# Kernel optimization log

Hardware: AMD Instinct MI355X
Metric: run time of the kernel (lower is better)

The kernel has to match this reference:

```python
import jax, jax.numpy as jnp
import numpy as np

HUMAN_SIZE = 54
NUM_ACTIONS = 15
INPUT_SIZE = HUMAN_SIZE + NUM_ACTIONS  # 69
RNN_SIZE = 2048
BATCH = 512
SRC_LEN = 100
TGT_LEN = 50


def setup_inputs() -> dict:
    key = jax.random.key(0)
    ks = jax.random.split(key, 8)
    s = 1.0 / np.sqrt(RNN_SIZE)
    return {
        "encoder_inputs": jax.random.normal(ks[0], (BATCH, SRC_LEN, INPUT_SIZE), jnp.float32),
        "decoder_inputs": jax.random.normal(ks[1], (BATCH, TGT_LEN, INPUT_SIZE), jnp.float32),
        # GRUCell params (torch layout: weight_ih [3H, D], weight_hh [3H, H])
        "W_ih": jax.random.uniform(ks[2], (3 * RNN_SIZE, INPUT_SIZE), jnp.float32, -s, s),
        "W_hh": jax.random.uniform(ks[3], (3 * RNN_SIZE, RNN_SIZE), jnp.float32, -s, s),
        "b_ih": jax.random.uniform(ks[4], (3 * RNN_SIZE,), jnp.float32, -s, s),
        "b_hh": jax.random.uniform(ks[5], (3 * RNN_SIZE,), jnp.float32, -s, s),
        # fc1: Linear(rnn_size -> input_size)
        "fc1_w": jax.random.uniform(ks[6], (INPUT_SIZE, RNN_SIZE), jnp.float32, -s, s),
        "fc1_b": jax.random.uniform(ks[7], (INPUT_SIZE,), jnp.float32, -s, s),
    }


def _gru_cell(x, h, W_ih, W_hh, b_ih, b_hh):
    # torch.nn.GRUCell math
    gi = x @ W_ih.T + b_ih  # [B, 3H]
    gh = h @ W_hh.T + b_hh  # [B, 3H]
    i_r, i_z, i_n = jnp.split(gi, 3, axis=-1)
    h_r, h_z, h_n = jnp.split(gh, 3, axis=-1)
    r = jax.nn.sigmoid(i_r + h_r)
    z = jax.nn.sigmoid(i_z + h_z)
    n = jnp.tanh(i_n + r * h_n)
    return (1.0 - z) * n + z * h


def reference(encoder_inputs, decoder_inputs, W_ih, W_hh, b_ih, b_hh, fc1_w, fc1_b):
    B = encoder_inputs.shape[0]
    state0 = jnp.zeros((B, RNN_SIZE), encoder_inputs.dtype)

    # Encoder: source_seq_len - 1 steps (dropout p=0.0 -> identity)
    enc_t = jnp.swapaxes(encoder_inputs[:, : SRC_LEN - 1], 0, 1)  # [L-1, B, D]

    def enc_step(h, x):
        return _gru_cell(x, h, W_ih, W_hh, b_ih, b_hh), None

    state, _ = jax.lax.scan(enc_step, state0, enc_t)

    # (loop_function feeds the previous output back as the next input).
    def dec_step(carry, _):
        h, inp = carry
        inp = jax.lax.stop_gradient(inp)  # inp.detach() in torch
        h = _gru_cell(inp, h, W_ih, W_hh, b_ih, b_hh)
        out = inp + h @ fc1_w.T + fc1_b  # residual
        return (h, out), out

    (_, _), outs = jax.lax.scan(dec_step, (state, decoder_inputs[:, 0]), None, length=TGT_LEN)
    return jnp.swapaxes(outs, 0, 1)  # [B, TGT_LEN, INPUT_SIZE]
```

## Files before the change

### kernel.cpp

```cpp
#include <hip/hip_runtime.h>

#define KP   2176
#define H    2048
#define MB   512
#define IN   69
#define TGT  50

typedef unsigned short ushort_t;
typedef __attribute__((ext_vector_type(8))) short  short8;
typedef __attribute__((ext_vector_type(4))) float  float4_t;

__device__ __forceinline__ ushort_t f2bf(float f) {
  union { float f; unsigned u; } v; v.f = f;
  unsigned u = v.u;
  return (ushort_t)((u + 0x7fffu + ((u >> 16) & 1u)) >> 16);
}

__device__ __forceinline__ void gload_lds16(const void* g, void* l) {
  __builtin_amdgcn_global_load_lds((const __attribute__((address_space(1))) void*)g,
                                   (__attribute__((address_space(3))) void*)l, 16, 0, 0);
}

template <int N> __device__ __forceinline__ void waitv() {
  asm volatile("s_waitcnt vmcnt(%0)" :: "n"(N) : "memory");
}


__global__ void build_wbig(const float* __restrict__ Whh, const float* __restrict__ Wih,
                           ushort_t* __restrict__ Wbig) {
  int k = blockIdx.x * 256 + threadIdx.x;
  int n = blockIdx.y;
  if (k >= KP) return;
  int g = (n >> 6) % 3;
  int c = (n / 192) * 64 + (n & 63);
  int gr = g * H + c;
  float v = 0.f;
  if (k < H) v = Whh[(size_t)gr * H + k];
  else if (k < H + IN) v = Wih[(size_t)gr * IN + (k - H)];
  Wbig[(size_t)n * KP + k] = f2bf(v);
}

__global__ void zero_u4(uint4* p, int n) {
  int i = blockIdx.x * 256 + threadIdx.x;
  if (i < n) p[i] = make_uint4(0, 0, 0, 0);
}

__global__ void fill_x0(const float* __restrict__ enc, ushort_t* __restrict__ Acat0) {
  int i = blockIdx.x * 256 + threadIdx.x;
  int b = i / IN, j = i - b * IN;
  Acat0[(size_t)b * KP + H + j] = f2bf(enc[(size_t)b * 100 * IN + j]);
}

__global__ void build_fc1(const float* __restrict__ fc1w, ushort_t* __restrict__ fc1b16) {
  int k = blockIdx.x * 256 + threadIdx.x;
  int n = blockIdx.y;
  float v = (n < IN) ? fc1w[(size_t)n * H + k] : 0.f;
  fc1b16[(size_t)n * H + k] = f2bf(v);
}

__global__ __launch_bounds__(256, 1) void gru_step(
    const ushort_t* __restrict__ Aprev, ushort_t* __restrict__ Anext,
    const ushort_t* __restrict__ Wbig, float* __restrict__ h32,
    const float* __restrict__ b_ih, const float* __restrict__ b_hh,
    const float* __restrict__ xsrc, int xstride)
{
  __shared__ __align__(16) char lds[4][32768];

  const int tid = threadIdx.x;
  const int bid = blockIdx.x;
  const int xcd = bid & 7, slot = bid >> 3;
  const int ct = xcd * 4 + (slot & 3);
  const int mt = slot >> 2;
  const int m0 = mt * 64, c0 = ct * 64;
  const int lane = tid & 63, w = tid >> 6;
  const int l15 = lane & 15, l4 = lane >> 4;

  const ushort_t* srcA[2];
  const ushort_t* srcB[6];
  #pragma unroll
  for (int r = 0; r < 2; ++r) {
    int byte = r * 4096 + tid * 16;
    int row = byte >> 7, colb = byte & 127;
    int sc = colb ^ ((row & 7) << 4);
    srcA[r] = Aprev + (size_t)(m0 + row) * KP + (sc >> 1);
  }
  #pragma unroll
  for (int r = 0; r < 6; ++r) {
    int byte = r * 4096 + tid * 16;
    int row = byte >> 7, colb = byte & 127;
    int sc = colb ^ ((row & 7) << 4);
    srcB[r] = Wbig + (size_t)(ct * 192 + row) * KP + (sc >> 1);
  }

  int offA[2][4], offB[2][3];
  #pragma unroll
  for (int kk = 0; kk < 2; ++kk) {
    int kbyte = kk * 64 + l4 * 16;
    #pragma unroll
    for (int mi = 0; mi < 4; ++mi) { int row = mi * 16 + l15; offA[kk][mi] = row * 128 + (kbyte ^ ((row & 7) << 4)); }
    #pragma unroll
    for (int ni = 0; ni < 3; ++ni) { int row = ni * 64 + w * 16 + l15; offB[kk][ni] = row * 128 + (kbyte ^ ((row & 7) << 4)); }
  }

  float4_t acc[4][4] = {};

  auto stage = [&](int kt, int buf) {
    const int kadv = kt * 64;
    char* base = &lds[0][0] + buf * 32768;
    #pragma unroll
    for (int r = 0; r < 2; ++r)
      gload_lds16(srcA[r] + kadv, base + r * 4096 + w * 1024);
    #pragma unroll
    for (int r = 0; r < 6; ++r)
      gload_lds16(srcB[r] + kadv, base + 8192 + r * 4096 + w * 1024);
  };

  auto compute = [&](int buf, bool g3) {
    const char* Ab = (const char*)&lds[0][0] + buf * 32768;
    const char* Bb = Ab + 8192;
    #pragma unroll
    for (int kk = 0; kk < 2; ++kk) {
      short8 a[4], b[3];
      #pragma unroll
      for (int mi = 0; mi < 4; ++mi) a[mi] = *(const short8*)(Ab + offA[kk][mi]);
      #pragma unroll
      for (int ni = 0; ni < 3; ++ni) b[ni] = *(const short8*)(Bb + offB[kk][ni]);
      #pragma unroll
      for (int mi = 0; mi < 4; ++mi) {
        acc[mi][0] = __builtin_amdgcn_mfma_f32_16x16x32_bf16(a[mi], b[0], acc[mi][0], 0, 0, 0);
        acc[mi][1] = __builtin_amdgcn_mfma_f32_16x16x32_bf16(a[mi], b[1], acc[mi][1], 0, 0, 0);
        if (!g3)
          acc[mi][2] = __builtin_amdgcn_mfma_f32_16x16x32_bf16(a[mi], b[2], acc[mi][2], 0, 0, 0);
        else
          acc[mi][3] = __builtin_amdgcn_mfma_f32_16x16x32_bf16(a[mi], b[2], acc[mi][3], 0, 0, 0);
      }
    }
  };

  #define BAR() __builtin_amdgcn_s_barrier()

  stage(0, 0); stage(1, 1); stage(2, 2);
  for (int kt = 0; kt < 28; kt += 4) {
    waitv<16>(); BAR(); compute(0, false); stage(kt + 3, 3);
    waitv<16>(); BAR(); compute(1, false); stage(kt + 4, 0);
    waitv<16>(); BAR(); compute(2, false); stage(kt + 5, 1);
    waitv<16>(); BAR(); compute(3, false); stage(kt + 6, 2);
  }
  waitv<16>(); BAR(); compute(0, false); stage(31, 3);
  waitv<16>(); BAR(); compute(1, false); stage(32, 0);
  waitv<16>(); BAR(); compute(2, false); stage(33, 1);
  waitv<16>(); BAR(); compute(3, false);
  waitv<8>();  BAR(); compute(0, true);
  waitv<0>();  BAR(); compute(1, true);

  const int c = c0 + w * 16 + l15;
  const float br  = b_ih[c] + b_hh[c];
  const float bz  = b_ih[H + c] + b_hh[H + c];
  const float bin = b_ih[2 * H + c];
  const float bhn = b_hh[2 * H + c];
  #pragma unroll
  for (int mi = 0; mi < 4; ++mi) {
    #pragma unroll
    for (int r4 = 0; r4 < 4; ++r4) {
      int m = m0 + mi * 16 + l4 * 4 + r4;
      float rg = 1.f / (1.f + __expf(-(acc[mi][0][r4] + br)));
      float zg = 1.f / (1.f + __expf(-(acc[mi][1][r4] + bz)));
      float ng = tanhf(acc[mi][3][r4] + bin + rg * (acc[mi][2][r4] + bhn));
      float hold = h32[(size_t)m * H + c];
      float hn = (1.f - zg) * ng + zg * hold;
      h32[(size_t)m * H + c] = hn;
      Anext[(size_t)m * KP + c] = f2bf(hn);
    }
  }
  if (ct == 0 && xsrc != nullptr) {
    for (int i = tid; i < 64 * IN; i += 256) {
      int rr = i / IN, cc = i - rr * IN;
      Anext[(size_t)(m0 + rr) * KP + H + cc] = f2bf(xsrc[(size_t)(m0 + rr) * xstride + cc]);
    }
  }
}

__global__ __launch_bounds__(256, 1) void out_step(
    ushort_t* Acat,
    const ushort_t* __restrict__ fc1b16,
    const float* __restrict__ fc1_bias,
    const float* __restrict__ inp,
    float* __restrict__ outp)
{
  __shared__ __align__(16) char lds[4][20480];
  const int tid = threadIdx.x;
  const int m0 = blockIdx.x * 64;
  const int lane = tid & 63, w = tid >> 6, l15 = lane & 15, l4 = lane >> 4;

  const ushort_t* srcA[2]; const ushort_t* srcB[3];
  #pragma unroll
  for (int r = 0; r < 2; ++r) {
    int byte = r * 4096 + tid * 16; int row = byte >> 7, colb = byte & 127;
    int sc = colb ^ ((row & 7) << 4);
    srcA[r] = Acat + (size_t)(m0 + row) * KP + (sc >> 1);
  }
  #pragma unroll
  for (int r = 0; r < 3; ++r) {
    int byte = r * 4096 + tid * 16; int row = byte >> 7, colb = byte & 127;
    int sc = colb ^ ((row & 7) << 4);
    srcB[r] = fc1b16 + (size_t)row * H + (sc >> 1);
  }
  int offA[2], offB[2][5];
  #pragma unroll
  for (int kk = 0; kk < 2; ++kk) {
    int kbyte = kk * 64 + l4 * 16;
    { int row = w * 16 + l15; offA[kk] = row * 128 + (kbyte ^ ((row & 7) << 4)); }
    #pragma unroll
    for (int ni = 0; ni < 5; ++ni) { int row = ni * 16 + l15; offB[kk][ni] = row * 128 + (kbyte ^ ((row & 7) << 4)); }
  }

  float4_t acc[5] = {};
  auto stage = [&](int kt, int buf) {
    int kadv = kt * 64;
    char* base = &lds[0][0] + buf * 20480;
    #pragma unroll
    for (int r = 0; r < 2; ++r) gload_lds16(srcA[r] + kadv, base + r * 4096 + w * 1024);
    #pragma unroll
    for (int r = 0; r < 3; ++r) gload_lds16(srcB[r] + kadv, base + 8192 + r * 4096 + w * 1024);
  };
  auto compute = [&](int buf) {
    const char* Ab = (const char*)&lds[0][0] + buf * 20480;
    const char* Bb = Ab + 8192;
    #pragma unroll
    for (int kk = 0; kk < 2; ++kk) {
      short8 a = *(const short8*)(Ab + offA[kk]);
      #pragma unroll
      for (int ni = 0; ni < 5; ++ni) {
        short8 b = *(const short8*)(Bb + offB[kk][ni]);
        acc[ni] = __builtin_amdgcn_mfma_f32_16x16x32_bf16(a, b, acc[ni], 0, 0, 0);
      }
    }
  };

  stage(0, 0); stage(1, 1); stage(2, 2);
  for (int kt = 0; kt < 28; kt += 4) {
    waitv<10>(); BAR(); compute(0); stage(kt + 3, 3);
    waitv<10>(); BAR(); compute(1); stage(kt + 4, 0);
    waitv<10>(); BAR(); compute(2); stage(kt + 5, 1);
    waitv<10>(); BAR(); compute(3); stage(kt + 6, 2);
  }
  waitv<10>(); BAR(); compute(0); stage(31, 3);
  waitv<10>(); BAR(); compute(1);
  waitv<5>();  BAR(); compute(2);
  waitv<0>();  BAR(); compute(3);

  #pragma unroll
  for (int ni = 0; ni < 5; ++ni) {
    int j = ni * 16 + l15;
    if (j < IN) {
      float bj = fc1_bias[j];
      #pragma unroll
      for (int r4 = 0; r4 < 4; ++r4) {
        int m = m0 + w * 16 + l4 * 4 + r4;
        float v = acc[ni][r4] + bj + inp[(size_t)m * (TGT * IN) + j];
        outp[(size_t)m * (TGT * IN) + j] = v;
        Acat[(size_t)m * KP + H + j] = f2bf(v);
      }
    }
  }
}

extern "C" void kernel_launch(void* const* d_in, const int* in_sizes, int n_in,
                              void* d_out, int out_size, void* d_ws, size_t ws_size,
                              hipStream_t stream) {
  const float* enc  = (const float*)d_in[0];
  const float* dec  = (const float*)d_in[1];
  const float* Wih  = (const float*)d_in[2];
  const float* Whh  = (const float*)d_in[3];
  const float* b_ih = (const float*)d_in[4];
  const float* b_hh = (const float*)d_in[5];
  const float* fc1w = (const float*)d_in[6];
  const float* fc1b = (const float*)d_in[7];
  float* out = (float*)d_out;

  char* ws = (char*)d_ws;
  ushort_t* Wbig   = (ushort_t*)(ws);
  ushort_t* Acat0  = (ushort_t*)(ws + 26738688);
  ushort_t* Acat1  = (ushort_t*)(ws + 28966912);
  float*    h32    = (float*)   (ws + 31195136);
  ushort_t* fc1b16 = (ushort_t*)(ws + 35389440);
  ushort_t* Acat[2] = {Acat0, Acat1};

  build_wbig<<<dim3(9, 6144), 256, 0, stream>>>(Whh, Wih, Wbig);
  zero_u4<<<2112, 256, 0, stream>>>((uint4*)Acat0, 540672);
  fill_x0<<<138, 256, 0, stream>>>(enc, Acat0);
  build_fc1<<<dim3(8, 96), 256, 0, stream>>>(fc1w, fc1b16);

  for (int t = 0; t < 149; ++t) {
    const float* xsrc = nullptr; int xstride = 0;
    if (t < 98)       { xsrc = enc + (size_t)(t + 1) * IN; xstride = 100 * IN; }
    else if (t == 98) { xsrc = dec;                        xstride = TGT * IN; }
    gru_step<<<256, 256, 0, stream>>>(Acat[t & 1], Acat[(t + 1) & 1], Wbig, h32,
                                      b_ih, b_hh, xsrc, xstride);
    if (t >= 99) {
      int d = t - 99;
      const float* inp = (d == 0) ? dec : out + (size_t)(d - 1) * IN;
      out_step<<<8, 256, 0, stream>>>(Acat[(t + 1) & 1], fc1b16, fc1b, inp,
                                      out + (size_t)d * IN);
    }
  }
}
```

Measured before the change: 4.275 ms.

## Retile GRU step to 128x96 blocks with register double-buffered fragments

Changes the per-block tile from 64 rows by 192 gate columns to 128 rows by 96 gate columns, with waves split 2x2 over the M and column dimensions, and reorders the packed weight layout to match. The LDS pipeline now prefetches MFMA fragments into two register sets, so LDS reads for the next k-tile overlap the MFMAs of the current one, with an explicit lgkmcnt wait before each barrier. The aim is a more balanced A/B load ratio per block and hiding LDS read latency. In exchange it uses more registers and tightens the pipeline's wait counts.

Result: no change. 4.354 ms (+1.8%).

```diff
diff --git a/kernel.cpp b/kernel.cpp
--- a/kernel.cpp
+++ b/kernel.cpp
@@ -2,7 +2,6 @@
 
 #define KP   2176
 #define H    2048
-#define MB   512
 #define IN   69
 #define TGT  50
 
@@ -24,6 +23,8 @@
 template <int N> __device__ __forceinline__ void waitv() {
   asm volatile("s_waitcnt vmcnt(%0)" :: "n"(N) : "memory");
 }
+#define LGKM0() asm volatile("s_waitcnt lgkmcnt(0)" ::: "memory")
+#define BAR()   __builtin_amdgcn_s_barrier()
 
 
 __global__ void build_wbig(const float* __restrict__ Whh, const float* __restrict__ Wih,
@@ -31,9 +32,9 @@
   int k = blockIdx.x * 256 + threadIdx.x;
   int n = blockIdx.y;
   if (k >= KP) return;
-  int g = (n >> 6) % 3;
-  int c = (n / 192) * 64 + (n & 63);
-  int gr = g * H + c;
+  int ct = n / 96, rem = n - ct * 96;
+  int g = rem >> 5, c32 = rem & 31;
+  int gr = g * H + ct * 32 + c32;
   float v = 0.f;
   if (k < H) v = Whh[(size_t)gr * H + k];
   else if (k < H + IN) v = Wih[(size_t)gr * IN + (k - H)];
@@ -57,6 +58,8 @@
   float v = (n < IN) ? fc1w[(size_t)n * H + k] : 0.f;
   fc1b16[(size_t)n * H + k] = f2bf(v);
 }
+
+struct Frag { short8 a[2][4]; short8 b[2][3]; };
 
 __global__ __launch_bounds__(256, 1) void gru_step(
     const ushort_t* __restrict__ Aprev, ushort_t* __restrict__ Anext,
@@ -64,32 +67,33 @@
     const float* __restrict__ b_ih, const float* __restrict__ b_hh,
     const float* __restrict__ xsrc, int xstride)
 {
-  __shared__ __align__(16) char lds[4][32768];
+  __shared__ __align__(16) char lds[4][28672];
 
   const int tid = threadIdx.x;
   const int bid = blockIdx.x;
   const int xcd = bid & 7, slot = bid >> 3;
-  const int ct = xcd * 4 + (slot & 3);
-  const int mt = slot >> 2;
-  const int m0 = mt * 64, c0 = ct * 64;
+  const int ct = xcd * 8 + (slot & 7);
+  const int mt = slot >> 3;
+  const int m0 = mt * 128;
   const int lane = tid & 63, w = tid >> 6;
   const int l15 = lane & 15, l4 = lane >> 4;
-
-  const ushort_t* srcA[2];
-  const ushort_t* srcB[6];
-  #pragma unroll
-  for (int r = 0; r < 2; ++r) {
+  const int wm = w & 1, wc = w >> 1;
+
+  const ushort_t* srcA[4];
+  const ushort_t* srcB[3];
+  #pragma unroll
+  for (int r = 0; r < 4; ++r) {
     int byte = r * 4096 + tid * 16;
     int row = byte >> 7, colb = byte & 127;
     int sc = colb ^ ((row & 7) << 4);
     srcA[r] = Aprev + (size_t)(m0 + row) * KP + (sc >> 1);
   }
   #pragma unroll
-  for (int r = 0; r < 6; ++r) {
+  for (int r = 0; r < 3; ++r) {
     int byte = r * 4096 + tid * 16;
     int row = byte >> 7, colb = byte & 127;
     int sc = colb ^ ((row & 7) << 4);
-    srcB[r] = Wbig + (size_t)(ct * 192 + row) * KP + (sc >> 1);
+    srcB[r] = Wbig + (size_t)(ct * 96 + row) * KP + (sc >> 1);
   }
 
   int offA[2][4], offB[2][3];
@@ -97,63 +101,81 @@
   for (int kk = 0; kk < 2; ++kk) {
     int kbyte = kk * 64 + l4 * 16;
     #pragma unroll
-    for (int mi = 0; mi < 4; ++mi) { int row = mi * 16 + l15; offA[kk][mi] = row * 128 + (kbyte ^ ((row & 7) << 4)); }
-    #pragma unroll
-    for (int ni = 0; ni < 3; ++ni) { int row = ni * 64 + w * 16 + l15; offB[kk][ni] = row * 128 + (kbyte ^ ((row & 7) << 4)); }
+    for (int mi = 0; mi < 4; ++mi) {
+      int row = wm * 64 + mi * 16 + l15;
+      offA[kk][mi] = row * 128 + (kbyte ^ ((row & 7) << 4));
+    }
+    #pragma unroll
+    for (int g = 0; g < 3; ++g) {
+      int row = g * 32 + wc * 16 + l15;
+      offB[kk][g] = 16384 + row * 128 + (kbyte ^ ((row & 7) << 4));
+    }
   }
 
   float4_t acc[4][4] = {};
+  Frag F0, F1;
 
   auto stage = [&](int kt, int buf) {
     const int kadv = kt * 64;
-    char* base = &lds[0][0] + buf * 32768;
-    #pragma unroll
-    for (int r = 0; r < 2; ++r)
+    char* base = &lds[0][0] + buf * 28672;
+    #pragma unroll
+    for (int r = 0; r < 4; ++r)
       gload_lds16(srcA[r] + kadv, base + r * 4096 + w * 1024);
     #pragma unroll
-    for (int r = 0; r < 6; ++r)
-      gload_lds16(srcB[r] + kadv, base + 8192 + r * 4096 + w * 1024);
-  };
-
-  auto compute = [&](int buf, bool g3) {
-    const char* Ab = (const char*)&lds[0][0] + buf * 32768;
-    const char* Bb = Ab + 8192;
+    for (int r = 0; r < 3; ++r)
+      gload_lds16(srcB[r] + kadv, base + 16384 + r * 4096 + w * 1024);
+  };
+
+  auto dsread = [&](Frag& f, int buf) {
+    const char* base = (const char*)&lds[0][0] + buf * 28672;
     #pragma unroll
     for (int kk = 0; kk < 2; ++kk) {
-      short8 a[4], b[3];
-      #pragma unroll
-      for (int mi = 0; mi < 4; ++mi) a[mi] = *(const short8*)(Ab + offA[kk][mi]);
-      #pragma unroll
-      for (int ni = 0; ni < 3; ++ni) b[ni] = *(const short8*)(Bb + offB[kk][ni]);
+      #pragma unroll
+      for (int mi = 0; mi < 4; ++mi) f.a[kk][mi] = *(const short8*)(base + offA[kk][mi]);
+      #pragma unroll
+      for (int g = 0; g < 3; ++g)   f.b[kk][g]  = *(const short8*)(base + offB[kk][g]);
+    }
+  };
+
+  auto domfma = [&](Frag& f, int g3) {
+    #pragma unroll
+    for (int kk = 0; kk < 2; ++kk) {
       #pragma unroll
       for (int mi = 0; mi < 4; ++mi) {
-        acc[mi][0] = __builtin_amdgcn_mfma_f32_16x16x32_bf16(a[mi], b[0], acc[mi][0], 0, 0, 0);
-        acc[mi][1] = __builtin_amdgcn_mfma_f32_16x16x32_bf16(a[mi], b[1], acc[mi][1], 0, 0, 0);
+        acc[mi][0] = __builtin_amdgcn_mfma_f32_16x16x32_bf16(f.a[kk][mi], f.b[kk][0], acc[mi][0], 0, 0, 0);
+        acc[mi][1] = __builtin_amdgcn_mfma_f32_16x16x32_bf16(f.a[kk][mi], f.b[kk][1], acc[mi][1], 0, 0, 0);
         if (!g3)
-          acc[mi][2] = __builtin_amdgcn_mfma_f32_16x16x32_bf16(a[mi], b[2], acc[mi][2], 0, 0, 0);
+          acc[mi][2] = __builtin_amdgcn_mfma_f32_16x16x32_bf16(f.a[kk][mi], f.b[kk][2], acc[mi][2], 0, 0, 0);
         else
-          acc[mi][3] = __builtin_amdgcn_mfma_f32_16x16x32_bf16(a[mi], b[2], acc[mi][3], 0, 0, 0);
+          acc[mi][3] = __builtin_amdgcn_mfma_f32_16x16x32_bf16(f.a[kk][mi], f.b[kk][2], acc[mi][3], 0, 0, 0);
       }
     }
   };
 
-  #define BAR() __builtin_amdgcn_s_barrier()
-
   stage(0, 0); stage(1, 1); stage(2, 2);
-  for (int kt = 0; kt < 28; kt += 4) {
-    waitv<16>(); BAR(); compute(0, false); stage(kt + 3, 3);
-    waitv<16>(); BAR(); compute(1, false); stage(kt + 4, 0);
-    waitv<16>(); BAR(); compute(2, false); stage(kt + 5, 1);
-    waitv<16>(); BAR(); compute(3, false); stage(kt + 6, 2);
-  }
-  waitv<16>(); BAR(); compute(0, false); stage(31, 3);
-  waitv<16>(); BAR(); compute(1, false); stage(32, 0);
-  waitv<16>(); BAR(); compute(2, false); stage(33, 1);
-  waitv<16>(); BAR(); compute(3, false);
-  waitv<8>();  BAR(); compute(0, true);
-  waitv<0>();  BAR(); compute(1, true);
-
-  const int c = c0 + w * 16 + l15;
+  waitv<14>(); LGKM0(); BAR();
+  dsread(F0, 0);
+
+  for (int i = 0; i < 30; i += 2) {
+    stage(i + 3, (i + 3) & 3);
+    waitv<14>(); LGKM0(); BAR();
+    dsread(F1, (i + 1) & 3);
+    domfma(F0, 0);
+    stage(i + 4, (i + 4) & 3);
+    waitv<14>(); LGKM0(); BAR();
+    dsread(F0, (i + 2) & 3);
+    domfma(F1, 0);
+  }
+  stage(33, 1);
+  waitv<14>(); LGKM0(); BAR();
+  dsread(F1, 3); domfma(F0, 0);
+  waitv<7>();  LGKM0(); BAR();
+  dsread(F0, 0); domfma(F1, 0);
+  waitv<0>();  LGKM0(); BAR();
+  dsread(F1, 1); domfma(F0, 1);
+  domfma(F1, 1);
+
+  const int c = ct * 32 + wc * 16 + l15;
   const float br  = b_ih[c] + b_hh[c];
   const float bz  = b_ih[H + c] + b_hh[H + c];
   const float bin = b_ih[2 * H + c];
@@ -162,7 +184,7 @@
   for (int mi = 0; mi < 4; ++mi) {
     #pragma unroll
     for (int r4 = 0; r4 < 4; ++r4) {
-      int m = m0 + mi * 16 + l4 * 4 + r4;
+      int m = m0 + wm * 64 + mi * 16 + l4 * 4 + r4;
       float rg = 1.f / (1.f + __expf(-(acc[mi][0][r4] + br)));
       float zg = 1.f / (1.f + __expf(-(acc[mi][1][r4] + bz)));
       float ng = tanhf(acc[mi][3][r4] + bin + rg * (acc[mi][2][r4] + bhn));
@@ -173,7 +195,7 @@
     }
   }
   if (ct == 0 && xsrc != nullptr) {
-    for (int i = tid; i < 64 * IN; i += 256) {
+    for (int i = tid; i < 128 * IN; i += 256) {
       int rr = i / IN, cc = i - rr * IN;
       Anext[(size_t)(m0 + rr) * KP + H + cc] = f2bf(xsrc[(size_t)(m0 + rr) * xstride + cc]);
     }
```

## Pre-swizzle weights and activations into MFMA fragment layout, load directly to registers

Applied to the files above, without the earlier changes.

Weights, fc1 weights and the activation buffers are stored in a pre-tiled layout that matches the MFMA operand fragments. This lets each lane load its short8 operand straight from global memory into registers, so the LDS staging via global_load_lds is dropped. The gru_step tile changes from 64x64 columns to 128 rows by 32 columns per block, with a 4-deep register prefetch. Dropping LDS removes the shared staging and bank-conflict work, but there is no longer any cross-wave operand reuse, so more L2 traffic and more vector registers are needed.

Result: slower. 5.037 ms (+17.8%).

```diff
diff --git a/kernel.cpp b/kernel.cpp
--- a/kernel.cpp
+++ b/kernel.cpp
@@ -2,9 +2,9 @@
 
 #define KP   2176
 #define H    2048
-#define MB   512
 #define IN   69
 #define TGT  50
+#define NKT  68
 
 typedef unsigned short ushort_t;
 typedef __attribute__((ext_vector_type(8))) short  short8;
@@ -16,28 +16,51 @@
   return (ushort_t)((u + 0x7fffu + ((u >> 16) & 1u)) >> 16);
 }
 
-__device__ __forceinline__ void gload_lds16(const void* g, void* l) {
-  __builtin_amdgcn_global_load_lds((const __attribute__((address_space(1))) void*)g,
-                                   (__attribute__((address_space(3))) void*)l, 16, 0, 0);
-}
-
 template <int N> __device__ __forceinline__ void waitv() {
   asm volatile("s_waitcnt vmcnt(%0)" :: "n"(N) : "memory");
 }
-
-
-__global__ void build_wbig(const float* __restrict__ Whh, const float* __restrict__ Wih,
-                           ushort_t* __restrict__ Wbig) {
-  int k = blockIdx.x * 256 + threadIdx.x;
-  int n = blockIdx.y;
-  if (k >= KP) return;
-  int g = (n >> 6) % 3;
-  int c = (n / 192) * 64 + (n & 63);
+#define BAR() __builtin_amdgcn_s_barrier()
+
+
+__global__ void build_w2(const float* __restrict__ Whh, const float* __restrict__ Wih,
+                         ushort_t* __restrict__ W2) {
+  int i = blockIdx.x * 256 + threadIdx.x;
+  int lane = i & 63;
+  int wc = (i >> 6) & 1;
+  int g  = (i >> 7) % 3;
+  int kt = (i / 384) % NKT;
+  int ct = i / 26112;
+  int c  = ct * 32 + wc * 16 + (lane & 15);
   int gr = g * H + c;
-  float v = 0.f;
-  if (k < H) v = Whh[(size_t)gr * H + k];
-  else if (k < H + IN) v = Wih[(size_t)gr * IN + (k - H)];
-  Wbig[(size_t)n * KP + k] = f2bf(v);
+  int k0 = kt * 32 + (lane >> 4) * 8;
+  ushort_t v[8];
+  #pragma unroll
+  for (int j = 0; j < 8; ++j) {
+    int k = k0 + j;
+    float val = 0.f;
+    if (k < H) val = Whh[(size_t)gr * H + k];
+    else if (k < H + IN) val = Wih[(size_t)gr * IN + (k - H)];
+    v[j] = f2bf(val);
+  }
+  #pragma unroll
+  for (int j = 0; j < 8; ++j) W2[(size_t)i * 8 + j] = v[j];
+}
+
+__global__ void build_f2(const float* __restrict__ fc1w, ushort_t* __restrict__ F2) {
+  int i = blockIdx.x * 256 + threadIdx.x;
+  int lane = i & 63;
+  int ni = (i >> 6) % 5;
+  int kt = i / 320;
+  int j  = ni * 16 + (lane & 15);
+  int k0 = kt * 32 + (lane >> 4) * 8;
+  ushort_t v[8];
+  #pragma unroll
+  for (int jj = 0; jj < 8; ++jj) {
+    float val = (j < IN) ? fc1w[(size_t)j * H + k0 + jj] : 0.f;
+    v[jj] = f2bf(val);
+  }
+  #pragma unroll
+  for (int jj = 0; jj < 8; ++jj) F2[(size_t)i * 8 + jj] = v[jj];
 }
 
 __global__ void zero_u4(uint4* p, int n) {
@@ -45,209 +68,150 @@
   if (i < n) p[i] = make_uint4(0, 0, 0, 0);
 }
 
-__global__ void fill_x0(const float* __restrict__ enc, ushort_t* __restrict__ Acat0) {
+__device__ __forceinline__ size_t a2_x_off(int b, int j) {
+  int k = 2048 + j;
+  int kt = k >> 5, kk = k & 31;
+  int mb = b >> 4;
+  int ln = (b & 15) | ((kk >> 3) << 4);
+  return ((size_t)(mb * NKT + kt) * 64 + ln) * 16 + (kk & 7) * 2;
+}
+
+__global__ void fill_x0(const float* __restrict__ enc, char* __restrict__ A2) {
   int i = blockIdx.x * 256 + threadIdx.x;
   int b = i / IN, j = i - b * IN;
-  Acat0[(size_t)b * KP + H + j] = f2bf(enc[(size_t)b * 100 * IN + j]);
-}
-
-__global__ void build_fc1(const float* __restrict__ fc1w, ushort_t* __restrict__ fc1b16) {
-  int k = blockIdx.x * 256 + threadIdx.x;
-  int n = blockIdx.y;
-  float v = (n < IN) ? fc1w[(size_t)n * H + k] : 0.f;
-  fc1b16[(size_t)n * H + k] = f2bf(v);
+  *(ushort_t*)(A2 + a2_x_off(b, j)) = f2bf(enc[(size_t)b * 100 * IN + j]);
 }
 
 __global__ __launch_bounds__(256, 1) void gru_step(
-    const ushort_t* __restrict__ Aprev, ushort_t* __restrict__ Anext,
-    const ushort_t* __restrict__ Wbig, float* __restrict__ h32,
+    const char* __restrict__ Aprev, char* __restrict__ Anext,
+    const char* __restrict__ W2, float* __restrict__ h32,
     const float* __restrict__ b_ih, const float* __restrict__ b_hh,
     const float* __restrict__ xsrc, int xstride)
 {
-  __shared__ __align__(16) char lds[4][32768];
-
   const int tid = threadIdx.x;
   const int bid = blockIdx.x;
   const int xcd = bid & 7, slot = bid >> 3;
-  const int ct = xcd * 4 + (slot & 3);
-  const int mt = slot >> 2;
-  const int m0 = mt * 64, c0 = ct * 64;
+  const int ct = xcd * 8 + (slot & 7);
+  const int mt = slot >> 3;
   const int lane = tid & 63, w = tid >> 6;
   const int l15 = lane & 15, l4 = lane >> 4;
-
-  const ushort_t* srcA[2];
-  const ushort_t* srcB[6];
-  #pragma unroll
-  for (int r = 0; r < 2; ++r) {
-    int byte = r * 4096 + tid * 16;
-    int row = byte >> 7, colb = byte & 127;
-    int sc = colb ^ ((row & 7) << 4);
-    srcA[r] = Aprev + (size_t)(m0 + row) * KP + (sc >> 1);
-  }
-  #pragma unroll
-  for (int r = 0; r < 6; ++r) {
-    int byte = r * 4096 + tid * 16;
-    int row = byte >> 7, colb = byte & 127;
-    int sc = colb ^ ((row & 7) << 4);
-    srcB[r] = Wbig + (size_t)(ct * 192 + row) * KP + (sc >> 1);
-  }
-
-  int offA[2][4], offB[2][3];
-  #pragma unroll
-  for (int kk = 0; kk < 2; ++kk) {
-    int kbyte = kk * 64 + l4 * 16;
-    #pragma unroll
-    for (int mi = 0; mi < 4; ++mi) { int row = mi * 16 + l15; offA[kk][mi] = row * 128 + (kbyte ^ ((row & 7) << 4)); }
-    #pragma unroll
-    for (int ni = 0; ni < 3; ++ni) { int row = ni * 64 + w * 16 + l15; offB[kk][ni] = row * 128 + (kbyte ^ ((row & 7) << 4)); }
-  }
-
+  const int wm = w & 1, wc = w >> 1;
+
+  const char* Ap[4];
+  #pragma unroll
+  for (int mi = 0; mi < 4; ++mi)
+    Ap[mi] = Aprev + ((size_t)(mt * 8 + wm * 4 + mi) * NKT) * 1024 + lane * 16;
+  const char* Bp[3];
+  #pragma unroll
+  for (int g = 0; g < 3; ++g)
+    Bp[g] = W2 + ((size_t)(ct * NKT) * 6 + g * 2 + wc) * 1024 + lane * 16;
+
+  short8 fa[4][4], fb[4][3];
   float4_t acc[4][4] = {};
 
-  auto stage = [&](int kt, int buf) {
-    const int kadv = kt * 64;
-    char* base = &lds[0][0] + buf * 32768;
-    #pragma unroll
-    for (int r = 0; r < 2; ++r)
-      gload_lds16(srcA[r] + kadv, base + r * 4096 + w * 1024);
-    #pragma unroll
-    for (int r = 0; r < 6; ++r)
-      gload_lds16(srcB[r] + kadv, base + 8192 + r * 4096 + w * 1024);
-  };
-
-  auto compute = [&](int buf, bool g3) {
-    const char* Ab = (const char*)&lds[0][0] + buf * 32768;
-    const char* Bb = Ab + 8192;
-    #pragma unroll
-    for (int kk = 0; kk < 2; ++kk) {
-      short8 a[4], b[3];
-      #pragma unroll
-      for (int mi = 0; mi < 4; ++mi) a[mi] = *(const short8*)(Ab + offA[kk][mi]);
-      #pragma unroll
-      for (int ni = 0; ni < 3; ++ni) b[ni] = *(const short8*)(Bb + offB[kk][ni]);
-      #pragma unroll
-      for (int mi = 0; mi < 4; ++mi) {
-        acc[mi][0] = __builtin_amdgcn_mfma_f32_16x16x32_bf16(a[mi], b[0], acc[mi][0], 0, 0, 0);
-        acc[mi][1] = __builtin_amdgcn_mfma_f32_16x16x32_bf16(a[mi], b[1], acc[mi][1], 0, 0, 0);
-        if (!g3)
-          acc[mi][2] = __builtin_amdgcn_mfma_f32_16x16x32_bf16(a[mi], b[2], acc[mi][2], 0, 0, 0);
-        else
-          acc[mi][3] = __builtin_amdgcn_mfma_f32_16x16x32_bf16(a[mi], b[2], acc[mi][3], 0, 0, 0);
-      }
-    }
-  };
-
-  #define BAR() __builtin_amdgcn_s_barrier()
-
-  stage(0, 0); stage(1, 1); stage(2, 2);
-  for (int kt = 0; kt < 28; kt += 4) {
-    waitv<16>(); BAR(); compute(0, false); stage(kt + 3, 3);
-    waitv<16>(); BAR(); compute(1, false); stage(kt + 4, 0);
-    waitv<16>(); BAR(); compute(2, false); stage(kt + 5, 1);
-    waitv<16>(); BAR(); compute(3, false); stage(kt + 6, 2);
-  }
-  waitv<16>(); BAR(); compute(0, false); stage(31, 3);
-  waitv<16>(); BAR(); compute(1, false); stage(32, 0);
-  waitv<16>(); BAR(); compute(2, false); stage(33, 1);
-  waitv<16>(); BAR(); compute(3, false);
-  waitv<8>();  BAR(); compute(0, true);
-  waitv<0>();  BAR(); compute(1, true);
-
-  const int c = c0 + w * 16 + l15;
+#define LOADT(d, kt) \
+  fa[d][0] = *(const short8*)(Ap[0] + (kt) * 1024); \
+  fa[d][1] = *(const short8*)(Ap[1] + (kt) * 1024); \
+  fa[d][2] = *(const short8*)(Ap[2] + (kt) * 1024); \
+  fa[d][3] = *(const short8*)(Ap[3] + (kt) * 1024); \
+  fb[d][0] = *(const short8*)(Bp[0] + (kt) * 6144); \
+  fb[d][1] = *(const short8*)(Bp[1] + (kt) * 6144); \
+  fb[d][2] = *(const short8*)(Bp[2] + (kt) * 6144);
+
+#define MFMAT(d, G2) \
+  { _Pragma("unroll") \
+    for (int mi = 0; mi < 4; ++mi) { \
+      acc[mi][0]  = __builtin_amdgcn_mfma_f32_16x16x32_bf16(fa[d][mi], fb[d][0], acc[mi][0], 0, 0, 0); \
+      acc[mi][1]  = __builtin_amdgcn_mfma_f32_16x16x32_bf16(fa[d][mi], fb[d][1], acc[mi][1], 0, 0, 0); \
+      acc[mi][G2] = __builtin_amdgcn_mfma_f32_16x16x32_bf16(fa[d][mi], fb[d][2], acc[mi][G2], 0, 0, 0); \
+    } }
+
+#define PROC(d, kt) { waitv<21>(); BAR(); MFMAT(d, 2); LOADT(d, (kt) + 4); }
+
+  LOADT(0, 0); LOADT(1, 1); LOADT(2, 2); LOADT(3, 3);
+  for (int kt = 0; kt < 64; kt += 4) {
+    PROC(0, kt); PROC(1, kt + 1); PROC(2, kt + 2); PROC(3, kt + 3);
+  }
+  waitv<21>(); BAR(); MFMAT(0, 3);
+  waitv<14>(); BAR(); MFMAT(1, 3);
+  waitv<7>();  BAR(); MFMAT(2, 3);
+  waitv<0>();  BAR(); MFMAT(3, 3);
+
+  const int c = ct * 32 + wc * 16 + l15;
   const float br  = b_ih[c] + b_hh[c];
   const float bz  = b_ih[H + c] + b_hh[H + c];
   const float bin = b_ih[2 * H + c];
   const float bhn = b_hh[2 * H + c];
+  const int ktc = c >> 5;
+  const int laneHi = ((c >> 3) & 3) << 4;
+  const int byteOff = (c & 7) * 2;
   #pragma unroll
   for (int mi = 0; mi < 4; ++mi) {
+    const int mb = mt * 8 + wm * 4 + mi;
+    char* dst = Anext + ((size_t)(mb * NKT + ktc) * 64 + laneHi) * 16 + byteOff;
     #pragma unroll
     for (int r4 = 0; r4 < 4; ++r4) {
-      int m = m0 + mi * 16 + l4 * 4 + r4;
+      int mlo = l4 * 4 + r4;
+      int m = mt * 128 + wm * 64 + mi * 16 + mlo;
       float rg = 1.f / (1.f + __expf(-(acc[mi][0][r4] + br)));
       float zg = 1.f / (1.f + __expf(-(acc[mi][1][r4] + bz)));
       float ng = tanhf(acc[mi][3][r4] + bin + rg * (acc[mi][2][r4] + bhn));
       float hold = h32[(size_t)m * H + c];
       float hn = (1.f - zg) * ng + zg * hold;
       h32[(size_t)m * H + c] = hn;
-      Anext[(size_t)m * KP + c] = f2bf(hn);
+      *(ushort_t*)(dst + mlo * 16) = f2bf(hn);
     }
   }
   if (ct == 0 && xsrc != nullptr) {
-    for (int i = tid; i < 64 * IN; i += 256) {
+    for (int i = tid; i < 128 * IN; i += 256) {
       int rr = i / IN, cc = i - rr * IN;
-      Anext[(size_t)(m0 + rr) * KP + H + cc] = f2bf(xsrc[(size_t)(m0 + rr) * xstride + cc]);
+      int b = mt * 128 + rr;
+      *(ushort_t*)(Anext + a2_x_off(b, cc)) = f2bf(xsrc[(size_t)b * xstride + cc]);
     }
   }
 }
 
 __global__ __launch_bounds__(256, 1) void out_step(
-    ushort_t* Acat,
-    const ushort_t* __restrict__ fc1b16,
+    char* Acat,
+    const char* __restrict__ F2,
     const float* __restrict__ fc1_bias,
     const float* __restrict__ inp,
     float* __restrict__ outp)
 {
-  __shared__ __align__(16) char lds[4][20480];
   const int tid = threadIdx.x;
-  const int m0 = blockIdx.x * 64;
-  const int lane = tid & 63, w = tid >> 6, l15 = lane & 15, l4 = lane >> 4;
-
-  const ushort_t* srcA[2]; const ushort_t* srcB[3];
-  #pragma unroll
-  for (int r = 0; r < 2; ++r) {
-    int byte = r * 4096 + tid * 16; int row = byte >> 7, colb = byte & 127;
-    int sc = colb ^ ((row & 7) << 4);
-    srcA[r] = Acat + (size_t)(m0 + row) * KP + (sc >> 1);
-  }
-  #pragma unroll
-  for (int r = 0; r < 3; ++r) {
-    int byte = r * 4096 + tid * 16; int row = byte >> 7, colb = byte & 127;
-    int sc = colb ^ ((row & 7) << 4);
-    srcB[r] = fc1b16 + (size_t)row * H + (sc >> 1);
-  }
-  int offA[2], offB[2][5];
-  #pragma unroll
-  for (int kk = 0; kk < 2; ++kk) {
-    int kbyte = kk * 64 + l4 * 16;
-    { int row = w * 16 + l15; offA[kk] = row * 128 + (kbyte ^ ((row & 7) << 4)); }
-    #pragma unroll
-    for (int ni = 0; ni < 5; ++ni) { int row = ni * 16 + l15; offB[kk][ni] = row * 128 + (kbyte ^ ((row & 7) << 4)); }
-  }
-
+  const int lane = tid & 63, w = tid >> 6;
+  const int l15 = lane & 15, l4 = lane >> 4;
+  const int mb = blockIdx.x * 4 + w;
+
+  const char* Ap = Acat + (size_t)mb * NKT * 1024 + lane * 16;
+  const char* Bp = F2 + lane * 16;
+
+  short8 fa[4]; short8 fb[4][5];
   float4_t acc[5] = {};
-  auto stage = [&](int kt, int buf) {
-    int kadv = kt * 64;
-    char* base = &lds[0][0] + buf * 20480;
-    #pragma unroll
-    for (int r = 0; r < 2; ++r) gload_lds16(srcA[r] + kadv, base + r * 4096 + w * 1024);
-    #pragma unroll
-    for (int r = 0; r < 3; ++r) gload_lds16(srcB[r] + kadv, base + 8192 + r * 4096 + w * 1024);
-  };
-  auto compute = [&](int buf) {
-    const char* Ab = (const char*)&lds[0][0] + buf * 20480;
-    const char* Bb = Ab + 8192;
-    #pragma unroll
-    for (int kk = 0; kk < 2; ++kk) {
-      short8 a = *(const short8*)(Ab + offA[kk]);
-      #pragma unroll
-      for (int ni = 0; ni < 5; ++ni) {
-        short8 b = *(const short8*)(Bb + offB[kk][ni]);
-        acc[ni] = __builtin_amdgcn_mfma_f32_16x16x32_bf16(a, b, acc[ni], 0, 0, 0);
-      }
-    }
-  };
-
-  stage(0, 0); stage(1, 1); stage(2, 2);
-  for (int kt = 0; kt < 28; kt += 4) {
-    waitv<10>(); BAR(); compute(0); stage(kt + 3, 3);
-    waitv<10>(); BAR(); compute(1); stage(kt + 4, 0);
-    waitv<10>(); BAR(); compute(2); stage(kt + 5, 1);
-    waitv<10>(); BAR(); compute(3); stage(kt + 6, 2);
-  }
-  waitv<10>(); BAR(); compute(0); stage(31, 3);
-  waitv<10>(); BAR(); compute(1);
-  waitv<5>();  BAR(); compute(2);
-  waitv<0>();  BAR(); compute(3);
+
+#define OLOAD(d, kt) \
+  fa[d]    = *(const short8*)(Ap + (kt) * 1024); \
+  fb[d][0] = *(const short8*)(Bp + (kt) * 5120); \
+  fb[d][1] = *(const short8*)(Bp + (kt) * 5120 + 1024); \
+  fb[d][2] = *(const short8*)(Bp + (kt) * 5120 + 2048); \
+  fb[d][3] = *(const short8*)(Bp + (kt) * 5120 + 3072); \
+  fb[d][4] = *(const short8*)(Bp + (kt) * 5120 + 4096);
+
+#define OMFMA(d) \
+  { _Pragma("unroll") \
+    for (int ni = 0; ni < 5; ++ni) \
+      acc[ni] = __builtin_amdgcn_mfma_f32_16x16x32_bf16(fa[d], fb[d][ni], acc[ni], 0, 0, 0); }
+
+#define OPROC(d, kt) { waitv<18>(); OMFMA(d); OLOAD(d, (kt) + 4); }
+
+  OLOAD(0, 0); OLOAD(1, 1); OLOAD(2, 2); OLOAD(3, 3);
+  for (int kt = 0; kt < 60; kt += 4) {
+    OPROC(0, kt); OPROC(1, kt + 1); OPROC(2, kt + 2); OPROC(3, kt + 3);
+  }
+  waitv<18>(); OMFMA(0);
+  waitv<12>(); OMFMA(1);
+  waitv<6>();  OMFMA(2);
+  waitv<0>();  OMFMA(3);
 
   #pragma unroll
   for (int ni = 0; ni < 5; ++ni) {
@@ -256,10 +220,10 @@
       float bj = fc1_bias[j];
       #pragma unroll
       for (int r4 = 0; r4 < 4; ++r4) {
-        int m = m0 + w * 16 + l4 * 4 + r4;
+        int m = mb * 16 + l4 * 4 + r4;
         float v = acc[ni][r4] + bj + inp[(size_t)m * (TGT * IN) + j];
         outp[(size_t)m * (TGT * IN) + j] = v;
-        Acat[(size_t)m * KP + H + j] = f2bf(v);
+        *(ushort_t*)(Acat + a2_x_off(m, j)) = f2bf(v);
       }
     }
   }
@@ -279,28 +243,28 @@
   float* out = (float*)d_out;
 
   char* ws = (char*)d_ws;
-  ushort_t* Wbig   = (ushort_t*)(ws);
-  ushort_t* Acat0  = (ushort_t*)(ws + 26738688);
-  ushort_t* Acat1  = (ushort_t*)(ws + 28966912);
-  float*    h32    = (float*)   (ws + 31195136);
-  ushort_t* fc1b16 = (ushort_t*)(ws + 35389440);
-  ushort_t* Acat[2] = {Acat0, Acat1};
-
-  build_wbig<<<dim3(9, 6144), 256, 0, stream>>>(Whh, Wih, Wbig);
-  zero_u4<<<2112, 256, 0, stream>>>((uint4*)Acat0, 540672);
-  fill_x0<<<138, 256, 0, stream>>>(enc, Acat0);
-  build_fc1<<<dim3(8, 96), 256, 0, stream>>>(fc1w, fc1b16);
+  ushort_t* W2  = (ushort_t*)(ws);
+  char*     A2_0 = ws + 26738688;
+  char*     A2_1 = ws + 28966912;
+  float*    h32  = (float*)(ws + 31195136);
+  ushort_t* F2   = (ushort_t*)(ws + 35389440);
+  char* A2[2] = {A2_0, A2_1};
+
+  build_w2<<<6528, 256, 0, stream>>>(Whh, Wih, W2);
+  zero_u4<<<2112, 256, 0, stream>>>((uint4*)A2_0, 540672);
+  fill_x0<<<138, 256, 0, stream>>>(enc, A2_0);
+  build_f2<<<80, 256, 0, stream>>>(fc1w, F2);
 
   for (int t = 0; t < 149; ++t) {
     const float* xsrc = nullptr; int xstride = 0;
     if (t < 98)       { xsrc = enc + (size_t)(t + 1) * IN; xstride = 100 * IN; }
     else if (t == 98) { xsrc = dec;                        xstride = TGT * IN; }
-    gru_step<<<256, 256, 0, stream>>>(Acat[t & 1], Acat[(t + 1) & 1], Wbig, h32,
+    gru_step<<<256, 256, 0, stream>>>(A2[t & 1], A2[(t + 1) & 1], (const char*)W2, h32,
                                       b_ih, b_hh, xsrc, xstride);
     if (t >= 99) {
       int d = t - 99;
       const float* inp = (d == 0) ? dec : out + (size_t)(d - 1) * IN;
-      out_step<<<8, 256, 0, stream>>>(Acat[(t + 1) & 1], fc1b16, fc1b, inp,
+      out_step<<<8, 256, 0, stream>>>(A2[(t + 1) & 1], (const char*)F2, fc1b, inp,
                                       out + (size_t)d * IN);
     }
   }
```
